# Optimization experiments

Hardware: AMD Instinct MI355X
Metric: run time of the kernel (lower is better)

## Reference

```python
import jax, jax.numpy as jnp
import numpy as np

B, N, FOV = 64, 128, 9
CH = [3, 32, 64, 128]
FLAT = CH[-1] * FOV * FOV  # 10368
ENC = 128
K = 3
G1, G2 = 128, 128
A = 5
EPS = 1e-5


def setup_inputs() -> dict:
    key = jax.random.key(0)
    ks = jax.random.split(key, 24)
    d = {}
    d["states"] = jax.random.normal(ks[0], (B, N, 3, FOV, FOV), jnp.float32)
    d["gso"] = jax.random.uniform(ks[1], (B, N, N), jnp.float32)
    i = 2
    for l in range(3):
        cin, cout = CH[l], CH[l + 1]
        d[f"c{l+1}_w"] = jax.random.normal(ks[i], (cout, cin, 3, 3), jnp.float32) * 0.05; i += 1
        d[f"c{l+1}_b"] = jnp.zeros((cout,), jnp.float32)
        d[f"c{l+1}_g"] = jnp.ones((cout,), jnp.float32)
        d[f"c{l+1}_be"] = jnp.zeros((cout,), jnp.float32)
    d["enc_w"] = jax.random.normal(ks[i], (ENC, FLAT), jnp.float32) * (1.0 / np.sqrt(FLAT)); i += 1
    d["enc_b"] = jnp.zeros((ENC,), jnp.float32)
    d["g1_w"] = jax.random.normal(ks[i], (K, G1, ENC), jnp.float32) * (1.0 / np.sqrt(ENC * K)); i += 1
    d["g1_b"] = jnp.zeros((G1,), jnp.float32)
    d["g2_w"] = jax.random.normal(ks[i], (K, G2, G1), jnp.float32) * (1.0 / np.sqrt(G1 * K)); i += 1
    d["g2_b"] = jnp.zeros((G2,), jnp.float32)
    d["act_w"] = jax.random.normal(ks[i], (A, G2), jnp.float32) * (1.0 / np.sqrt(G2)); i += 1
    d["act_b"] = jnp.zeros((A,), jnp.float32)
    return d


def _conv_bn_relu(x, w, b, gamma, beta):
    # 3x3, stride 1, padding 1 -> SAME; NCHW/OIHW
    y = jax.lax.conv_general_dilated(
        x, w, window_strides=(1, 1), padding="SAME",
        dimension_numbers=("NCHW", "OIHW", "NCHW"))
    y = y + b[None, :, None, None]
    # BatchNorm2d in training mode: batch statistics over (N, H, W)
    mu = jnp.mean(y, axis=(0, 2, 3), keepdims=True)
    var = jnp.var(y, axis=(0, 2, 3), keepdims=True)
    y = (y - mu) * jax.lax.rsqrt(var + EPS)
    y = y * gamma[None, :, None, None] + beta[None, :, None, None]
    return jax.nn.relu(y)


def _graph_filter(x, S, w, b):
    # x: [B, F, N], S: [B, N, N], w: [K, G, F] -> y = sum_k W_k (x S^k) + b
    out = jnp.einsum("bfn,gf->bgn", x, w[0])
    xk = x
    for k in range(1, w.shape[0]):
        xk = jnp.einsum("bfn,bnm->bfm", xk, S)
        out = out + jnp.einsum("bfn,gf->bgn", xk, w[k])
    return out + b[None, :, None]


def reference(states, gso,
              c1_w, c1_b, c1_g, c1_be,
              c2_w, c2_b, c2_g, c2_be,
              c3_w, c3_b, c3_g, c3_be,
              enc_w, enc_b, g1_w, g1_b, g2_w, g2_b, act_w, act_b):
    x = states.reshape(B * N, 3, FOV, FOV)
    x = _conv_bn_relu(x, c1_w, c1_b, c1_g, c1_be)
    x = _conv_bn_relu(x, c2_w, c2_b, c2_g, c2_be)
    x = _conv_bn_relu(x, c3_w, c3_b, c3_g, c3_be)
    x = x.reshape(B * N, FLAT)
    x = x @ enc_w.T + enc_b                    # [B*N, ENC]
    x = x.reshape(B, N, ENC).transpose(0, 2, 1)  # [B, F, N]
    x = jax.nn.relu(_graph_filter(x, gso, g1_w, g1_b))
    x = jax.nn.relu(_graph_filter(x, gso, g2_w, g2_b))
    x = x.transpose(0, 2, 1).reshape(B * N, G2)
    logits = x @ act_w.T + act_b
    return logits.reshape(B, N, A)
```

## Files before the change

kernel.cpp:

```cpp
#include <hip/hip_runtime.h>
#include <hip/hip_bf16.h>
#include <stdint.h>


#define NIMG 8192
#define NPIX 81
#define FLAT 10368

typedef __hip_bfloat16 bf16;
typedef short bf16x8 __attribute__((ext_vector_type(8)));
typedef float f32x4 __attribute__((ext_vector_type(4)));

__device__ __forceinline__ float bflo(unsigned u) { return __uint_as_float(u << 16); }
__device__ __forceinline__ float bfhi(unsigned u) { return __uint_as_float(u & 0xffff0000u); }
__device__ __forceinline__ unsigned short f2bf(float f) {
    unsigned u = __float_as_uint(f);
    return (unsigned short)((u + 0x7fff + ((u >> 16) & 1)) >> 16);
}

__device__ __forceinline__ bf16x8 bn8(bf16x8 a, const float* sc, const float* sh) {
    union U { bf16x8 v; unsigned u[4]; } in, out;
    in.v = a;
#pragma unroll
    for (int d = 0; d < 4; d++) {
        float lo = fmaxf(fmaf(bflo(in.u[d]), sc[2 * d],     sh[2 * d]),     0.f);
        float hi = fmaxf(fmaf(bfhi(in.u[d]), sc[2 * d + 1], sh[2 * d + 1]), 0.f);
        out.u[d] = (unsigned)f2bf(lo) | ((unsigned)f2bf(hi) << 16);
    }
    return out.v;
}

__global__ void fill_sentinel(float* __restrict__ out, int n) {
    int i = blockIdx.x * 256 + threadIdx.x;
    if (i < n) out[i] = 1.0e9f;
}

__global__ void prep_w(const float* __restrict__ c1w, const float* __restrict__ c2w,
                       const float* __restrict__ c3w,
                       float* __restrict__ w1t, bf16* __restrict__ w2m,
                       bf16* __restrict__ w3m) {
    int i0 = blockIdx.x * blockDim.x + threadIdx.x;
    int stride = gridDim.x * blockDim.x;
    for (int i = i0; i < 27 * 32; i += stride) w1t[i] = c1w[(i & 31) * 27 + (i >> 5)];
    for (int i = i0; i < 64 * 288; i += stride) {
        int oc = i / 288, r = i - oc * 288, t = r >> 5, ci = r & 31;
        w2m[i] = __float2bfloat16(c2w[oc * 288 + ci * 9 + t]);
    }
    for (int i = i0; i < 128 * 576; i += stride) {
        int oc = i / 576, r = i - oc * 576, t = r >> 6, ci = r & 63;
        w3m[i] = __float2bfloat16(c3w[oc * 576 + ci * 9 + t]);
    }
}

__global__ void prep_enc(const float* __restrict__ encw, bf16* __restrict__ ewb) {
    int i0 = blockIdx.x * blockDim.x + threadIdx.x;
    int stride = gridDim.x * blockDim.x;
    for (int i = i0; i < 128 * FLAT; i += stride) {
        int e = i / FLAT, r = i - e * FLAT;
        int kk = r >> 5, c32 = r & 31;
        int px = kk >> 2, cc = kk & 3;
        ewb[i] = __float2bfloat16(encw[(size_t)e * FLAT + (cc * 32 + c32) * 81 + px]);
    }
}

template <int NCH>
__global__ __launch_bounds__(256) void bnrelu_k(bf16* __restrict__ x,
        const float* __restrict__ st, int n8) {
    int i0 = blockIdx.x * 256 + threadIdx.x;
    int stride = gridDim.x * 256;
    for (int i = i0; i < n8; i += stride) {
        size_t base = (size_t)i * 8;
        int ch = (int)((base >> 18) & (unsigned)(NCH - 1));
        int c0 = ch * 32 + (int)(base & 31);
        float sc[8], sh[8];
#pragma unroll
        for (int j = 0; j < 8; j++) {
            sc[j] = st[c0 + j];
            sh[j] = st[NCH * 32 + c0 + j];
        }
        bf16x8 v = *(bf16x8*)(x + base);
        *(bf16x8*)(x + base) = bn8(v, sc, sh);
    }
}

__device__ __forceinline__ void load_row(const float* __restrict__ p, float* r) {
    float4 a = *(const float4*)p;
    float4 b = *(const float4*)(p + 4);
    float4 c = *(const float4*)(p + 8);
    r[0]=a.x; r[1]=a.y; r[2]=a.z;  r[3]=a.w;
    r[4]=b.x; r[5]=b.y; r[6]=b.z;  r[7]=b.w;
    r[8]=c.x; r[9]=c.y; r[10]=c.z; r[11]=c.w;
}

__device__ __forceinline__ void conv_body(const float* __restrict__ inp,
                                          const float* __restrict__ wv, float* acc) {
    float rb[3][12];
    load_row(inp, rb[0]);
    load_row(inp + 12, rb[1]);
#pragma unroll
    for (int oy = 0; oy < 9; oy++) {
        load_row(inp + (oy + 2) * 12, rb[(oy + 2) % 3]);
#pragma unroll
        for (int ky = 0; ky < 3; ky++) {
            const float* r = rb[(oy + ky) % 3];
#pragma unroll
            for (int ox = 0; ox < 9; ox++) {
                float s = acc[oy * 9 + ox];
                s = fmaf(r[ox + 0], wv[ky * 3 + 0], s);
                s = fmaf(r[ox + 1], wv[ky * 3 + 1], s);
                s = fmaf(r[ox + 2], wv[ky * 3 + 2], s);
                acc[oy * 9 + ox] = s;
            }
        }
    }
}

__global__ __launch_bounds__(128) void conv1_kernel(const float* __restrict__ xin,
        const float* __restrict__ wt, const float* __restrict__ bias,
        bf16* __restrict__ xout, float* __restrict__ sacc) {
    __shared__ __align__(16) float lds[4 * 3 * 132];
    __shared__ float Sl[128], Ql[128];
    int t = threadIdx.x;
    int img0 = blockIdx.x * 4;
    for (int i = t; i < 4 * 3 * 132; i += 128) lds[i] = 0.f;
    __syncthreads();
    const float* src = xin + (size_t)img0 * 243;
    for (int i = t; i < 4 * 243; i += 128) {
        int il = i / 243, rem = i - il * 243;
        int ci = rem / 81, px = rem - ci * 81;
        lds[(il * 3 + ci) * 132 + (px / 9 + 1) * 12 + (px % 9) + 1] = src[i];
    }
    __syncthreads();
    int oc = t & 31, il = t >> 5;
    const float* base = lds + il * 3 * 132;
    float acc[81];
    float bb = bias[oc];
#pragma unroll
    for (int i = 0; i < 81; i++) acc[i] = bb;
#pragma unroll
    for (int ci = 0; ci < 3; ci++) {
        float wv[9];
#pragma unroll
        for (int k = 0; k < 9; k++) wv[k] = wt[(ci * 9 + k) * 32 + oc];
        conv_body(base + ci * 132, wv, acc);
    }
    bf16* dst = xout + (size_t)(img0 + il) * 32 + oc;
    const size_t PXS = (size_t)NIMG * 32;
    float s = 0.f, q = 0.f;
#pragma unroll
    for (int p = 0; p < 81; p++) {
        float v = acc[p];
        s += v; q = fmaf(v, v, q);
        dst[p * PXS] = __float2bfloat16(v);
    }
    Sl[il * 32 + oc] = s;
    Ql[il * 32 + oc] = q;
    __syncthreads();
    if (t < 32)
        atomicAdd(&sacc[t], Sl[t] + Sl[32 + t] + Sl[64 + t] + Sl[96 + t]);
    else if (t < 64) {
        int c = t - 32;
        atomicAdd(&sacc[32 + c], Ql[c] + Ql[32 + c] + Ql[64 + c] + Ql[96 + c]);
    }
}

template <int CI, int COT, int OCS>
__global__ __launch_bounds__(256, (CI == 64) ? 2 : 4) void conv_tile(
        const bf16* __restrict__ xin,
        const bf16* __restrict__ wm, const float* __restrict__ bias,
        bf16* __restrict__ xout, float* __restrict__ sacc) {
    constexpr int NCH = CI / 32;
    constexpr int NCHO = COT / 32;
    constexpr int NOC = COT / OCS;
    constexpr int NF = NOC / 16;
    constexpr int LNF = (NF == 8) ? 3 : 2;
    constexpr int ROW = 9 * CI;
    constexpr int STEPS = 9 * NCH;
    constexpr int PHASES = STEPS / 9;
    constexpr int HS = STEPS / PHASES;
    constexpr size_t CSTRIDE = (size_t)NIMG * 32;
    __shared__ bf16 Bs[HS * NF * 64 * 8];
    __shared__ float Ss[2][4][NOC];

    const int lin = blockIdx.x;
    const int xcd = lin & 7;
    const int slot = lin >> 3;
    constexpr int PSL = 81 * OCS;
    const int igl = slot / PSL;
    const int rem = slot - igl * PSL;
    const int p = rem / OCS;
    const int ob = rem - p * OCS;
    const int ig = xcd * 4 + igl;
    const int oc0 = ob * NOC;
    const int py = p / 9, pxx = p - py * 9;
    const int tid = threadIdx.x;
    const int lane = tid & 63, wv = tid >> 6;
    const int m = lane & 15, quad = lane >> 4;
    const long img0 = (long)ig * 256 + wv * 64;

    int qt[9]; bool vt[9];
#pragma unroll
    for (int t = 0; t < 9; t++) {
        int iy = py + t / 3 - 1, ix = pxx + (t % 3) - 1;
        vt[t] = ((unsigned)iy < 9u) && ((unsigned)ix < 9u);
        qt[t] = vt[t] ? iy * 9 + ix : p;
    }

    f32x4 acc[4][NF];
#pragma unroll
    for (int nf = 0; nf < NF; nf++) {
        float bb = bias[oc0 + nf * 16 + m];
#pragma unroll
        for (int ms = 0; ms < 4; ms++) {
            acc[ms][nf][0] = bb; acc[ms][nf][1] = bb;
            acc[ms][nf][2] = bb; acc[ms][nf][3] = bb;
        }
    }
    const bf16* ab[4];
#pragma unroll
    for (int ms = 0; ms < 4; ms++)
        ab[ms] = xin + (img0 + ms * 16 + m) * 32 + quad * 8;

    const bf16* bsl = &Bs[lane * 8];

#pragma unroll
    for (int ph = 0; ph < PHASES; ph++) {
        __syncthreads();
        for (int i = tid; i < HS * NF * 64; i += 256) {
            int l2 = i & 63, nf = (i >> 6) & (NF - 1), sl = i >> (6 + LNF);
            int s = ph * HS + sl;
            int t = s / NCH, ch = s - t * NCH;
            int mm = l2 & 15, qq = l2 >> 4;
            *(bf16x8*)(&Bs[(size_t)i * 8]) =
                *(const bf16x8*)(wm + (size_t)(oc0 + nf * 16 + mm) * ROW + t * CI + ch * 32 + qq * 8);
        }
        __syncthreads();
#pragma unroll
        for (int sl = 0; sl < HS; sl++) {
            const int s = ph * HS + sl;
            const int t = s / NCH, ch = s - t * NCH;
            if (vt[t]) {
                bf16x8 bfr[NF];
#pragma unroll
                for (int nf = 0; nf < NF; nf++)
                    bfr[nf] = *(const bf16x8*)(bsl + (sl * NF + nf) * 512);
                bf16x8 a[4];
#pragma unroll
                for (int ms = 0; ms < 4; ms++)
                    a[ms] = *(const bf16x8*)(ab[ms] + (size_t)(qt[t] * NCH + ch) * CSTRIDE);
#pragma unroll
                for (int ms = 0; ms < 4; ms++) {
#pragma unroll
                    for (int nf = 0; nf < NF; nf++)
                        acc[ms][nf] = __builtin_amdgcn_mfma_f32_16x16x32_bf16(a[ms], bfr[nf], acc[ms][nf], 0, 0, 0);
                }
            }
        }
    }

    const int och = oc0 >> 5;
#pragma unroll
    for (int ms = 0; ms < 4; ms++)
#pragma unroll
        for (int nf = 0; nf < NF; nf++) {
            bf16* orow = xout
                + (((size_t)p * NCHO + och + (nf >> 1)) * NIMG + img0 + ms * 16 + quad * 4) * 32
                + (nf & 1) * 16 + m;
#pragma unroll
            for (int r = 0; r < 4; r++)
                orow[r * 32] = __float2bfloat16(acc[ms][nf][r]);
        }

    float ssum[NF], sq[NF];
#pragma unroll
    for (int nf = 0; nf < NF; nf++) {
        float s = 0.f, q = 0.f;
#pragma unroll
        for (int ms = 0; ms < 4; ms++)
#pragma unroll
            for (int r = 0; r < 4; r++) {
                float v = acc[ms][nf][r];
                s += v; q = fmaf(v, v, q);
            }
        s += __shfl_xor(s, 16); s += __shfl_xor(s, 32);
        q += __shfl_xor(q, 16); q += __shfl_xor(q, 32);
        ssum[nf] = s; sq[nf] = q;
    }
    if (lane < 16) {
#pragma unroll
        for (int nf = 0; nf < NF; nf++) {
            Ss[0][wv][nf * 16 + lane] = ssum[nf];
            Ss[1][wv][nf * 16 + lane] = sq[nf];
        }
    }
    __syncthreads();
    if (tid < NOC) {
        float a = Ss[0][0][tid] + Ss[0][1][tid] + Ss[0][2][tid] + Ss[0][3][tid];
        atomicAdd(&sacc[oc0 + tid], a);
    } else if (tid < 2 * NOC) {
        int c = tid - NOC;
        float a = Ss[1][0][c] + Ss[1][1][c] + Ss[1][2][c] + Ss[1][3][c];
        atomicAdd(&sacc[COT + oc0 + c], a);
    }
}

__global__ __launch_bounds__(256) void enc_mfma(const bf16* __restrict__ x3,
        const bf16* __restrict__ ewb, const float* __restrict__ st,
        float* __restrict__ part) {
    const int lin = blockIdx.x;
    const int xcd = lin & 7;
    const int slot = lin >> 3;
    const int igl = slot >> 3;
    const int combo = slot & 7;
    const int ks = combo >> 1, nh = combo & 1;
    const int ig = xcd * 8 + igl;
    const int lane = threadIdx.x & 63, wv = threadIdx.x >> 6;
    const int m = lane & 15, quad = lane >> 4;
    const long img0 = (long)ig * 128 + wv * 32;
    constexpr size_t CSTRIDE = (size_t)NIMG * 32;

    float scv[4][8], shv[4][8];
#pragma unroll
    for (int cc = 0; cc < 4; cc++)
#pragma unroll
        for (int j = 0; j < 8; j++) {
            int ci = cc * 32 + quad * 8 + j;
            scv[cc][j] = st[ci];
            shv[cc][j] = st[128 + ci];
        }

    f32x4 acc[2][4];
#pragma unroll
    for (int ms = 0; ms < 2; ms++)
#pragma unroll
        for (int nf = 0; nf < 4; nf++) {
            acc[ms][nf][0]=0.f; acc[ms][nf][1]=0.f; acc[ms][nf][2]=0.f; acc[ms][nf][3]=0.f;
        }
    const bf16* ab[2];
    const bf16* bb[4];
#pragma unroll
    for (int ms = 0; ms < 2; ms++)
        ab[ms] = x3 + (size_t)(ks * 81) * CSTRIDE + (img0 + ms * 16 + m) * 32 + quad * 8;
#pragma unroll
    for (int nf = 0; nf < 4; nf++)
        bb[nf] = ewb + (size_t)(nh * 64 + nf * 16 + m) * FLAT + ks * 81 * 32 + quad * 8;

#pragma unroll 3
    for (int c = 0; c < 81; c++) {
        const int cc = (ks + c) & 3;
        bf16x8 Ac[2], Bc[4];
#pragma unroll
        for (int ms = 0; ms < 2; ms++) {
            bf16x8 raw = *(const bf16x8*)(ab[ms] + (size_t)c * CSTRIDE);
            Ac[ms] = bn8(raw, scv[cc], shv[cc]);
        }
#pragma unroll
        for (int nf = 0; nf < 4; nf++) Bc[nf] = *(const bf16x8*)(bb[nf] + c * 32);
#pragma unroll
        for (int nf = 0; nf < 4; nf++)
#pragma unroll
            for (int ms = 0; ms < 2; ms++)
                acc[ms][nf] = __builtin_amdgcn_mfma_f32_16x16x32_bf16(Ac[ms], Bc[nf], acc[ms][nf], 0, 0, 0);
    }

    float* pp = part + (size_t)ks * (NIMG * 128) + (img0 + quad * 4) * 128 + nh * 64 + m;
#pragma unroll
    for (int ms = 0; ms < 2; ms++)
#pragma unroll
        for (int nf = 0; nf < 4; nf++)
#pragma unroll
            for (int r = 0; r < 4; r++)
                pp[(ms * 16 + r) * 128 + nf * 16] = acc[ms][nf][r];
}

template <int CO>
__global__ void stats_fin(const float* __restrict__ acc, const float* __restrict__ gamma,
                          const float* __restrict__ beta, float* __restrict__ st) {
    int c = threadIdx.x;
    if (c < CO) {
        const float inv = 1.0f / (8192.0f * 81.0f);
        float m = acc[c] * inv;
        float var = acc[CO + c] * inv - m * m;
        float istd = rsqrtf(var + 1e-5f);
        float sc = istd * gamma[c];
        st[c] = sc;
        st[CO + c] = beta[c] - m * sc;
    }
}

__global__ void enc_reduce(const float* __restrict__ part, const float* __restrict__ encb,
                           float* __restrict__ xT) {
    int i = blockIdx.x * 256 + threadIdx.x;
    const int NP = NIMG * 128;
    if (i < NP) {
        float v = part[i] + part[NP + i] + part[2 * NP + i] + part[3 * NP + i] + encb[i & 127];
        int img = i >> 7, f = i & 127;
        xT[(size_t)(img >> 7) * 16384 + f * 128 + (img & 127)] = v;
    }
}

__global__ __launch_bounds__(256) void mm_xs(const float* __restrict__ A,
        const float* __restrict__ S, float* __restrict__ Y) {
    __shared__ __align__(16) float Sc[32 * 132];
    __shared__ float Acm[32 * 33];
    int b = blockIdx.y, f0 = blockIdx.x * 32;
    int t = threadIdx.x;
    int fl = t & 31, mg = t >> 5;
    const float* Ab = A + (size_t)b * 16384;
    const float* Sb = S + (size_t)b * 16384;
    float acc[16];
#pragma unroll
    for (int j = 0; j < 16; j++) acc[j] = 0.f;
    for (int nc = 0; nc < 128; nc += 32) {
#pragma unroll
        for (int r = 0; r < 4; r++) {
            int i4 = r * 256 + t;
            int nn = i4 >> 5, m4 = (i4 & 31) * 4;
            *(float4*)&Sc[nn * 132 + m4] = *(const float4*)&Sb[(size_t)(nc + nn) * 128 + m4];
        }
#pragma unroll
        for (int r = 0; r < 4; r++) {
            int i = r * 256 + t;
            int ff = i >> 5, nn = i & 31;
            Acm[ff * 33 + nn] = Ab[(size_t)(f0 + ff) * 128 + nc + nn];
        }
        __syncthreads();
#pragma unroll 4
        for (int nn = 0; nn < 32; nn++) {
            float a = Acm[fl * 33 + nn];
#pragma unroll
            for (int j = 0; j < 4; j++) {
                float4 s4 = *(const float4*)&Sc[nn * 132 + mg * 16 + j * 4];
                acc[j*4+0] = fmaf(a, s4.x, acc[j*4+0]);
                acc[j*4+1] = fmaf(a, s4.y, acc[j*4+1]);
                acc[j*4+2] = fmaf(a, s4.z, acc[j*4+2]);
                acc[j*4+3] = fmaf(a, s4.w, acc[j*4+3]);
            }
        }
        __syncthreads();
    }
    float* yb = Y + (size_t)b * 16384 + (size_t)(f0 + fl) * 128 + mg * 16;
#pragma unroll
    for (int j = 0; j < 4; j++)
        *(float4*)&yb[j * 4] = make_float4(acc[j*4], acc[j*4+1], acc[j*4+2], acc[j*4+3]);
}

__global__ __launch_bounds__(256) void gf_combine(const float* __restrict__ Z0,
        const float* __restrict__ Z1, const float* __restrict__ Z2,
        const float* __restrict__ W, const float* __restrict__ bias,
        float* __restrict__ out) {
    __shared__ __align__(16) float Zc[32 * 132];
    __shared__ float Wc[32 * 33];
    int b = blockIdx.y, g0 = blockIdx.x * 32;
    int t = threadIdx.x;
    int gl = t & 31, mg = t >> 5;
    float acc[16];
    float bb = bias[g0 + gl];
#pragma unroll
    for (int j = 0; j < 16; j++) acc[j] = bb;
    const float* Zs[3] = {Z0 + (size_t)b * 16384, Z1 + (size_t)b * 16384, Z2 + (size_t)b * 16384};
    for (int j3 = 0; j3 < 3; j3++) {
        const float* Zb = Zs[j3];
        const float* Wj = W + j3 * 16384;
        for (int fc = 0; fc < 128; fc += 32) {
#pragma unroll
            for (int r = 0; r < 4; r++) {
                int i4 = r * 256 + t;
                int ff = i4 >> 5, m4 = (i4 & 31) * 4;
                *(float4*)&Zc[ff * 132 + m4] = *(const float4*)&Zb[(size_t)(fc + ff) * 128 + m4];
            }
#pragma unroll
            for (int r = 0; r < 4; r++) {
                int i = r * 256 + t;
                int gg = i >> 5, ff = i & 31;
                Wc[gg * 33 + ff] = Wj[(size_t)(g0 + gg) * 128 + fc + ff];
            }
            __syncthreads();
#pragma unroll 4
            for (int ff = 0; ff < 32; ff++) {
                float w = Wc[gl * 33 + ff];
#pragma unroll
                for (int j = 0; j < 4; j++) {
                    float4 z4 = *(const float4*)&Zc[ff * 132 + mg * 16 + j * 4];
                    acc[j*4+0] = fmaf(w, z4.x, acc[j*4+0]);
                    acc[j*4+1] = fmaf(w, z4.y, acc[j*4+1]);
                    acc[j*4+2] = fmaf(w, z4.z, acc[j*4+2]);
                    acc[j*4+3] = fmaf(w, z4.w, acc[j*4+3]);
                }
            }
            __syncthreads();
        }
    }
    float* ob = out + (size_t)b * 16384 + (size_t)(g0 + gl) * 128 + mg * 16;
#pragma unroll
    for (int j = 0; j < 4; j++)
        *(float4*)&ob[j * 4] = make_float4(fmaxf(acc[j*4], 0.f), fmaxf(acc[j*4+1], 0.f),
                                           fmaxf(acc[j*4+2], 0.f), fmaxf(acc[j*4+3], 0.f));
}

__global__ __launch_bounds__(128) void act_kernel(const float* __restrict__ X,
        const float* __restrict__ aw, const float* __restrict__ ab,
        float* __restrict__ out) {
    int b = blockIdx.x, n = threadIdx.x;
    float acc[5];
#pragma unroll
    for (int a = 0; a < 5; a++) acc[a] = ab[a];
    const float* xb = X + (size_t)b * 16384 + n;
#pragma unroll 4
    for (int g = 0; g < 128; g++) {
        float v = xb[(size_t)g * 128];
#pragma unroll
        for (int a = 0; a < 5; a++) acc[a] = fmaf(v, aw[a * 128 + g], acc[a]);
    }
    float* ob = out + ((size_t)b * 128 + n) * 5;
#pragma unroll
    for (int a = 0; a < 5; a++) ob[a] = acc[a];
}

extern "C" void kernel_launch(void* const* d_in, const int* in_sizes, int n_in,
                              void* d_out, int out_size, void* d_ws, size_t ws_size,
                              hipStream_t stream) {
    const float* states = (const float*)d_in[0];
    const float* gso    = (const float*)d_in[1];
    const float* c1w  = (const float*)d_in[2];
    const float* c1b  = (const float*)d_in[3];
    const float* c1g  = (const float*)d_in[4];
    const float* c1be = (const float*)d_in[5];
    const float* c2w  = (const float*)d_in[6];
    const float* c2b  = (const float*)d_in[7];
    const float* c2g  = (const float*)d_in[8];
    const float* c2be = (const float*)d_in[9];
    const float* c3w  = (const float*)d_in[10];
    const float* c3b  = (const float*)d_in[11];
    const float* c3g  = (const float*)d_in[12];
    const float* c3be = (const float*)d_in[13];
    const float* encw = (const float*)d_in[14];
    const float* encb = (const float*)d_in[15];
    const float* g1w  = (const float*)d_in[16];
    const float* g1b  = (const float*)d_in[17];
    const float* g2w  = (const float*)d_in[18];
    const float* g2b  = (const float*)d_in[19];
    const float* aw   = (const float*)d_in[20];
    const float* ab   = (const float*)d_in[21];
    float* out = (float*)d_out;
    char* ws = (char*)d_ws;

    size_t o = 0;
    auto take = [&](size_t bytes) { size_t r = o; o += (bytes + 255) & ~(size_t)255; return r; };
    const size_t o_x3  = take((size_t)81 * 4 * NIMG * 32 * 2);
    const size_t o_x2  = take((size_t)81 * 2 * NIMG * 32 * 2);
    const size_t o_w1t = take(27 * 32 * 4);
    const size_t o_w2m = take(64 * 288 * 2);
    const size_t o_w3m = take(128 * 576 * 2);
    const size_t o_acc = take(448 * 4);
    const size_t o_st1 = take(2 * 32 * 4);
    const size_t o_st2 = take(2 * 64 * 4);
    const size_t o_st3 = take(2 * 128 * 4);
    if (ws_size < o) {
        fill_sentinel<<<(out_size + 255) / 256, 256, 0, stream>>>(out, out_size);
        return;
    }

    const size_t o_x1 = o_x3;
    const size_t o_ewb  = o_x2;
    const size_t o_part = o_x2 + 2654208;
    const size_t o_xT   = o_part + 16777216;
    const size_t o_y1   = o_xT + 4194304;
    const size_t o_y2   = o_y1 + 4194304;
    const size_t o_G1   = o_y2 + 4194304;
    const size_t o_G2   = o_G1 + 4194304;

    bf16* x1 = (bf16*)(ws + o_x1);
    bf16* x2 = (bf16*)(ws + o_x2);
    bf16* x3 = (bf16*)(ws + o_x3);
    float* w1t = (float*)(ws + o_w1t);
    bf16* w2m = (bf16*)(ws + o_w2m);
    bf16* w3m = (bf16*)(ws + o_w3m);
    float* acc1 = (float*)(ws + o_acc);
    float* acc2 = acc1 + 64;
    float* acc3 = acc1 + 192;
    float* st1 = (float*)(ws + o_st1);
    float* st2 = (float*)(ws + o_st2);
    float* st3 = (float*)(ws + o_st3);
    bf16* ewb = (bf16*)(ws + o_ewb);
    float* partp = (float*)(ws + o_part);
    float* xT = (float*)(ws + o_xT);
    float* y1 = (float*)(ws + o_y1);
    float* y2 = (float*)(ws + o_y2);
    float* xG1 = (float*)(ws + o_G1);
    float* xG2 = (float*)(ws + o_G2);

    hipMemsetAsync(ws + o_acc, 0, 448 * 4, stream);
    prep_w<<<128, 256, 0, stream>>>(c1w, c2w, c3w, w1t, w2m, w3m);

    conv1_kernel<<<2048, 128, 0, stream>>>(states, w1t, c1b, x1, acc1);
    stats_fin<32><<<1, 32, 0, stream>>>(acc1, c1g, c1be, st1);
    bnrelu_k<1><<<4096, 256, 0, stream>>>(x1, st1, 81 * 1 * NIMG * 32 / 8);

    conv_tile<32, 64, 1><<<2592, 256, 0, stream>>>(x1, w2m, c2b, x2, acc2);
    stats_fin<64><<<1, 64, 0, stream>>>(acc2, c2g, c2be, st2);
    bnrelu_k<2><<<4096, 256, 0, stream>>>(x2, st2, 81 * 2 * NIMG * 32 / 8);

    conv_tile<64, 128, 1><<<2592, 256, 0, stream>>>(x2, w3m, c3b, x3, acc3);
    stats_fin<128><<<1, 128, 0, stream>>>(acc3, c3g, c3be, st3);

    prep_enc<<<2048, 256, 0, stream>>>(encw, ewb);
    enc_mfma<<<512, 256, 0, stream>>>(x3, ewb, st3, partp);
    enc_reduce<<<4096, 256, 0, stream>>>(partp, encb, xT);

    mm_xs<<<dim3(4, 64), 256, 0, stream>>>(xT, gso, y1);
    mm_xs<<<dim3(4, 64), 256, 0, stream>>>(y1, gso, y2);
    gf_combine<<<dim3(4, 64), 256, 0, stream>>>(xT, y1, y2, g1w, g1b, xG1);

    mm_xs<<<dim3(4, 64), 256, 0, stream>>>(xG1, gso, y1);
    mm_xs<<<dim3(4, 64), 256, 0, stream>>>(y1, gso, y2);
    gf_combine<<<dim3(4, 64), 256, 0, stream>>>(xG1, y1, y2, g2w, g2b, xG2);

    act_kernel<<<64, 128, 0, stream>>>(xG2, aw, ab, out);
}
```

Baseline: 687.8 us.

## Fold BN stats finalize into consumers, retile encoder MFMA and graph matmuls

Removes the three single-block stats_fin launches by computing BN scale/shift inside bnrelu_k (via shared memory) and inside enc_mfma per thread. Retiles enc_mfma so each wave covers 16 images across all 128 output features instead of 32 images by 64 features, which drops the nh split. Halves the feature tile in mm_xs and gf_combine so twice as many blocks launch (512 instead of 256), aiming for better CU occupancy on small graph stages. The trade-off is redundant stats computation in every block and more B-operand loads per A load in the encoder.

```diff
diff --git a/kernel.cpp b/kernel.cpp
--- a/kernel.cpp
+++ b/kernel.cpp
@@ -65,8 +65,20 @@
 
 template <int NCH>
 __global__ __launch_bounds__(256) void bnrelu_k(bf16* __restrict__ x,
-        const float* __restrict__ st, int n8) {
-    int i0 = blockIdx.x * 256 + threadIdx.x;
+        const float* __restrict__ accp, const float* __restrict__ gma,
+        const float* __restrict__ bta, int n8) {
+    __shared__ float stl[2][NCH * 32];
+    int t = threadIdx.x;
+    if (t < NCH * 32) {
+        const float inv = 1.0f / (8192.0f * 81.0f);
+        float mean = accp[t] * inv;
+        float var = accp[NCH * 32 + t] * inv - mean * mean;
+        float sc = rsqrtf(var + 1e-5f) * gma[t];
+        stl[0][t] = sc;
+        stl[1][t] = bta[t] - mean * sc;
+    }
+    __syncthreads();
+    int i0 = blockIdx.x * 256 + t;
     int stride = gridDim.x * 256;
     for (int i = i0; i < n8; i += stride) {
         size_t base = (size_t)i * 8;
@@ -75,8 +87,8 @@
         float sc[8], sh[8];
 #pragma unroll
         for (int j = 0; j < 8; j++) {
-            sc[j] = st[c0 + j];
-            sh[j] = st[NCH * 32 + c0 + j];
+            sc[j] = stl[0][c0 + j];
+            sh[j] = stl[1][c0 + j];
         }
         bf16x8 v = *(bf16x8*)(x + base);
         *(bf16x8*)(x + base) = bn8(v, sc, sh);
@@ -305,87 +317,64 @@
 }
 
 __global__ __launch_bounds__(256) void enc_mfma(const bf16* __restrict__ x3,
-        const bf16* __restrict__ ewb, const float* __restrict__ st,
+        const bf16* __restrict__ ewb, const float* __restrict__ acc3,
+        const float* __restrict__ gma, const float* __restrict__ bta,
         float* __restrict__ part) {
     const int lin = blockIdx.x;
     const int xcd = lin & 7;
     const int slot = lin >> 3;
-    const int igl = slot >> 3;
-    const int combo = slot & 7;
-    const int ks = combo >> 1, nh = combo & 1;
-    const int ig = xcd * 8 + igl;
+    const int igl = slot >> 2;
+    const int ks = slot & 3;
+    const int ig = xcd * 16 + igl;
     const int lane = threadIdx.x & 63, wv = threadIdx.x >> 6;
     const int m = lane & 15, quad = lane >> 4;
-    const long img0 = (long)ig * 128 + wv * 32;
+    const long img0 = (long)ig * 64 + wv * 16;
     constexpr size_t CSTRIDE = (size_t)NIMG * 32;
 
+    const float inv = 1.0f / (8192.0f * 81.0f);
     float scv[4][8], shv[4][8];
 #pragma unroll
     for (int cc = 0; cc < 4; cc++)
 #pragma unroll
         for (int j = 0; j < 8; j++) {
             int ci = cc * 32 + quad * 8 + j;
-            scv[cc][j] = st[ci];
-            shv[cc][j] = st[128 + ci];
-        }
-
-    f32x4 acc[2][4];
-#pragma unroll
-    for (int ms = 0; ms < 2; ms++)
-#pragma unroll
-        for (int nf = 0; nf < 4; nf++) {
-            acc[ms][nf][0]=0.f; acc[ms][nf][1]=0.f; acc[ms][nf][2]=0.f; acc[ms][nf][3]=0.f;
-        }
-    const bf16* ab[2];
-    const bf16* bb[4];
-#pragma unroll
-    for (int ms = 0; ms < 2; ms++)
-        ab[ms] = x3 + (size_t)(ks * 81) * CSTRIDE + (img0 + ms * 16 + m) * 32 + quad * 8;
-#pragma unroll
-    for (int nf = 0; nf < 4; nf++)
-        bb[nf] = ewb + (size_t)(nh * 64 + nf * 16 + m) * FLAT + ks * 81 * 32 + quad * 8;
+            float mean = acc3[ci] * inv;
+            float var = acc3[128 + ci] * inv - mean * mean;
+            float sc = rsqrtf(var + 1e-5f) * gma[ci];
+            scv[cc][j] = sc;
+            shv[cc][j] = bta[ci] - mean * sc;
+        }
+
+    f32x4 acc[8];
+#pragma unroll
+    for (int nf = 0; nf < 8; nf++) {
+        acc[nf][0]=0.f; acc[nf][1]=0.f; acc[nf][2]=0.f; acc[nf][3]=0.f;
+    }
+    const bf16* ab = x3 + (size_t)(ks * 81) * CSTRIDE + (img0 + m) * 32 + quad * 8;
+    const bf16* bb[8];
+#pragma unroll
+    for (int nf = 0; nf < 8; nf++)
+        bb[nf] = ewb + (size_t)(nf * 16 + m) * FLAT + ks * 81 * 32 + quad * 8;
 
 #pragma unroll 3
     for (int c = 0; c < 81; c++) {
         const int cc = (ks + c) & 3;
-        bf16x8 Ac[2], Bc[4];
-#pragma unroll
-        for (int ms = 0; ms < 2; ms++) {
-            bf16x8 raw = *(const bf16x8*)(ab[ms] + (size_t)c * CSTRIDE);
-            Ac[ms] = bn8(raw, scv[cc], shv[cc]);
-        }
-#pragma unroll
-        for (int nf = 0; nf < 4; nf++) Bc[nf] = *(const bf16x8*)(bb[nf] + c * 32);
-#pragma unroll
-        for (int nf = 0; nf < 4; nf++)
-#pragma unroll
-            for (int ms = 0; ms < 2; ms++)
-                acc[ms][nf] = __builtin_amdgcn_mfma_f32_16x16x32_bf16(Ac[ms], Bc[nf], acc[ms][nf], 0, 0, 0);
-    }
-
-    float* pp = part + (size_t)ks * (NIMG * 128) + (img0 + quad * 4) * 128 + nh * 64 + m;
-#pragma unroll
-    for (int ms = 0; ms < 2; ms++)
-#pragma unroll
-        for (int nf = 0; nf < 4; nf++)
-#pragma unroll
-            for (int r = 0; r < 4; r++)
-                pp[(ms * 16 + r) * 128 + nf * 16] = acc[ms][nf][r];
-}
-
-template <int CO>
-__global__ void stats_fin(const float* __restrict__ acc, const float* __restrict__ gamma,
-                          const float* __restrict__ beta, float* __restrict__ st) {
-    int c = threadIdx.x;
-    if (c < CO) {
-        const float inv = 1.0f / (8192.0f * 81.0f);
-        float m = acc[c] * inv;
-        float var = acc[CO + c] * inv - m * m;
-        float istd = rsqrtf(var + 1e-5f);
-        float sc = istd * gamma[c];
-        st[c] = sc;
-        st[CO + c] = beta[c] - m * sc;
-    }
+        bf16x8 raw = *(const bf16x8*)(ab + (size_t)c * CSTRIDE);
+        bf16x8 Ac = bn8(raw, scv[cc], shv[cc]);
+        bf16x8 Bc[8];
+#pragma unroll
+        for (int nf = 0; nf < 8; nf++) Bc[nf] = *(const bf16x8*)(bb[nf] + c * 32);
+#pragma unroll
+        for (int nf = 0; nf < 8; nf++)
+            acc[nf] = __builtin_amdgcn_mfma_f32_16x16x32_bf16(Ac, Bc[nf], acc[nf], 0, 0, 0);
+    }
+
+    float* pp = part + (size_t)ks * (NIMG * 128) + (img0 + quad * 4) * 128 + m;
+#pragma unroll
+    for (int nf = 0; nf < 8; nf++)
+#pragma unroll
+        for (int r = 0; r < 4; r++)
+            pp[r * 128 + nf * 16] = acc[nf][r];
 }
 
 __global__ void enc_reduce(const float* __restrict__ part, const float* __restrict__ encb,
@@ -402,15 +391,15 @@
 __global__ __launch_bounds__(256) void mm_xs(const float* __restrict__ A,
         const float* __restrict__ S, float* __restrict__ Y) {
     __shared__ __align__(16) float Sc[32 * 132];
-    __shared__ float Acm[32 * 33];
-    int b = blockIdx.y, f0 = blockIdx.x * 32;
+    __shared__ float Acm[16 * 33];
+    int b = blockIdx.y, f0 = blockIdx.x * 16;
     int t = threadIdx.x;
-    int fl = t & 31, mg = t >> 5;
+    int fl = t & 15, mg = t >> 4;
     const float* Ab = A + (size_t)b * 16384;
     const float* Sb = S + (size_t)b * 16384;
-    float acc[16];
-#pragma unroll
-    for (int j = 0; j < 16; j++) acc[j] = 0.f;
+    float acc[8];
+#pragma unroll
+    for (int j = 0; j < 8; j++) acc[j] = 0.f;
     for (int nc = 0; nc < 128; nc += 32) {
 #pragma unroll
         for (int r = 0; r < 4; r++) {
@@ -419,7 +408,7 @@
             *(float4*)&Sc[nn * 132 + m4] = *(const float4*)&Sb[(size_t)(nc + nn) * 128 + m4];
         }
 #pragma unroll
-        for (int r = 0; r < 4; r++) {
+        for (int r = 0; r < 2; r++) {
             int i = r * 256 + t;
             int ff = i >> 5, nn = i & 31;
             Acm[ff * 33 + nn] = Ab[(size_t)(f0 + ff) * 128 + nc + nn];
@@ -429,8 +418,8 @@
         for (int nn = 0; nn < 32; nn++) {
             float a = Acm[fl * 33 + nn];
 #pragma unroll
-            for (int j = 0; j < 4; j++) {
-                float4 s4 = *(const float4*)&Sc[nn * 132 + mg * 16 + j * 4];
+            for (int j = 0; j < 2; j++) {
+                float4 s4 = *(const float4*)&Sc[nn * 132 + mg * 8 + j * 4];
                 acc[j*4+0] = fmaf(a, s4.x, acc[j*4+0]);
                 acc[j*4+1] = fmaf(a, s4.y, acc[j*4+1]);
                 acc[j*4+2] = fmaf(a, s4.z, acc[j*4+2]);
@@ -439,10 +428,9 @@
         }
         __syncthreads();
     }
-    float* yb = Y + (size_t)b * 16384 + (size_t)(f0 + fl) * 128 + mg * 16;
-#pragma unroll
-    for (int j = 0; j < 4; j++)
-        *(float4*)&yb[j * 4] = make_float4(acc[j*4], acc[j*4+1], acc[j*4+2], acc[j*4+3]);
+    float* yb = Y + (size_t)b * 16384 + (size_t)(f0 + fl) * 128 + mg * 8;
+    *(float4*)&yb[0] = make_float4(acc[0], acc[1], acc[2], acc[3]);
+    *(float4*)&yb[4] = make_float4(acc[4], acc[5], acc[6], acc[7]);
 }
 
 __global__ __launch_bounds__(256) void gf_combine(const float* __restrict__ Z0,
@@ -450,14 +438,14 @@
         const float* __restrict__ W, const float* __restrict__ bias,
         float* __restrict__ out) {
     __shared__ __align__(16) float Zc[32 * 132];
-    __shared__ float Wc[32 * 33];
-    int b = blockIdx.y, g0 = blockIdx.x * 32;
+    __shared__ float Wc[16 * 33];
+    int b = blockIdx.y, g0 = blockIdx.x * 16;
     int t = threadIdx.x;
-    int gl = t & 31, mg = t >> 5;
-    float acc[16];
+    int gl = t & 15, mg = t >> 4;
+    float acc[8];
     float bb = bias[g0 + gl];
 #pragma unroll
-    for (int j = 0; j < 16; j++) acc[j] = bb;
+    for (int j = 0; j < 8; j++) acc[j] = bb;
     const float* Zs[3] = {Z0 + (size_t)b * 16384, Z1 + (size_t)b * 16384, Z2 + (size_t)b * 16384};
     for (int j3 = 0; j3 < 3; j3++) {
         const float* Zb = Zs[j3];
@@ -470,7 +458,7 @@
                 *(float4*)&Zc[ff * 132 + m4] = *(const float4*)&Zb[(size_t)(fc + ff) * 128 + m4];
             }
 #pragma unroll
-            for (int r = 0; r < 4; r++) {
+            for (int r = 0; r < 2; r++) {
                 int i = r * 256 + t;
                 int gg = i >> 5, ff = i & 31;
                 Wc[gg * 33 + ff] = Wj[(size_t)(g0 + gg) * 128 + fc + ff];
@@ -480,8 +468,8 @@
             for (int ff = 0; ff < 32; ff++) {
                 float w = Wc[gl * 33 + ff];
 #pragma unroll
-                for (int j = 0; j < 4; j++) {
-                    float4 z4 = *(const float4*)&Zc[ff * 132 + mg * 16 + j * 4];
+                for (int j = 0; j < 2; j++) {
+                    float4 z4 = *(const float4*)&Zc[ff * 132 + mg * 8 + j * 4];
                     acc[j*4+0] = fmaf(w, z4.x, acc[j*4+0]);
                     acc[j*4+1] = fmaf(w, z4.y, acc[j*4+1]);
                     acc[j*4+2] = fmaf(w, z4.z, acc[j*4+2]);
@@ -491,11 +479,11 @@
             __syncthreads();
         }
     }
-    float* ob = out + (size_t)b * 16384 + (size_t)(g0 + gl) * 128 + mg * 16;
-#pragma unroll
-    for (int j = 0; j < 4; j++)
-        *(float4*)&ob[j * 4] = make_float4(fmaxf(acc[j*4], 0.f), fmaxf(acc[j*4+1], 0.f),
-                                           fmaxf(acc[j*4+2], 0.f), fmaxf(acc[j*4+3], 0.f));
+    float* ob = out + (size_t)b * 16384 + (size_t)(g0 + gl) * 128 + mg * 8;
+    *(float4*)&ob[0] = make_float4(fmaxf(acc[0], 0.f), fmaxf(acc[1], 0.f),
+                                   fmaxf(acc[2], 0.f), fmaxf(acc[3], 0.f));
+    *(float4*)&ob[4] = make_float4(fmaxf(acc[4], 0.f), fmaxf(acc[5], 0.f),
+                                   fmaxf(acc[6], 0.f), fmaxf(acc[7], 0.f));
 }
 
 __global__ __launch_bounds__(128) void act_kernel(const float* __restrict__ X,
@@ -553,9 +541,6 @@
     const size_t o_w2m = take(64 * 288 * 2);
     const size_t o_w3m = take(128 * 576 * 2);
     const size_t o_acc = take(448 * 4);
-    const size_t o_st1 = take(2 * 32 * 4);
-    const size_t o_st2 = take(2 * 64 * 4);
-    const size_t o_st3 = take(2 * 128 * 4);
     if (ws_size < o) {
         fill_sentinel<<<(out_size + 255) / 256, 256, 0, stream>>>(out, out_size);
         return;
@@ -579,9 +564,6 @@
     float* acc1 = (float*)(ws + o_acc);
     float* acc2 = acc1 + 64;
     float* acc3 = acc1 + 192;
-    float* st1 = (float*)(ws + o_st1);
-    float* st2 = (float*)(ws + o_st2);
-    float* st3 = (float*)(ws + o_st3);
     bf16* ewb = (bf16*)(ws + o_ewb);
     float* partp = (float*)(ws + o_part);
     float* xT = (float*)(ws + o_xT);
@@ -594,27 +576,24 @@
     prep_w<<<128, 256, 0, stream>>>(c1w, c2w, c3w, w1t, w2m, w3m);
 
     conv1_kernel<<<2048, 128, 0, stream>>>(states, w1t, c1b, x1, acc1);
-    stats_fin<32><<<1, 32, 0, stream>>>(acc1, c1g, c1be, st1);
-    bnrelu_k<1><<<4096, 256, 0, stream>>>(x1, st1, 81 * 1 * NIMG * 32 / 8);
+    bnrelu_k<1><<<4096, 256, 0, stream>>>(x1, acc1, c1g, c1be, 81 * 1 * NIMG * 32 / 8);
 
     conv_tile<32, 64, 1><<<2592, 256, 0, stream>>>(x1, w2m, c2b, x2, acc2);
-    stats_fin<64><<<1, 64, 0, stream>>>(acc2, c2g, c2be, st2);
-    bnrelu_k<2><<<4096, 256, 0, stream>>>(x2, st2, 81 * 2 * NIMG * 32 / 8);
+    bnrelu_k<2><<<4096, 256, 0, stream>>>(x2, acc2, c2g, c2be, 81 * 2 * NIMG * 32 / 8);
 
     conv_tile<64, 128, 1><<<2592, 256, 0, stream>>>(x2, w3m, c3b, x3, acc3);
-    stats_fin<128><<<1, 128, 0, stream>>>(acc3, c3g, c3be, st3);
 
     prep_enc<<<2048, 256, 0, stream>>>(encw, ewb);
-    enc_mfma<<<512, 256, 0, stream>>>(x3, ewb, st3, partp);
+    enc_mfma<<<512, 256, 0, stream>>>(x3, ewb, acc3, c3g, c3be, partp);
     enc_reduce<<<4096, 256, 0, stream>>>(partp, encb, xT);
 
-    mm_xs<<<dim3(4, 64), 256, 0, stream>>>(xT, gso, y1);
-    mm_xs<<<dim3(4, 64), 256, 0, stream>>>(y1, gso, y2);
-    gf_combine<<<dim3(4, 64), 256, 0, stream>>>(xT, y1, y2, g1w, g1b, xG1);
-
-    mm_xs<<<dim3(4, 64), 256, 0, stream>>>(xG1, gso, y1);
-    mm_xs<<<dim3(4, 64), 256, 0, stream>>>(y1, gso, y2);
-    gf_combine<<<dim3(4, 64), 256, 0, stream>>>(xG1, y1, y2, g2w, g2b, xG2);
+    mm_xs<<<dim3(8, 64), 256, 0, stream>>>(xT, gso, y1);
+    mm_xs<<<dim3(8, 64), 256, 0, stream>>>(y1, gso, y2);
+    gf_combine<<<dim3(8, 64), 256, 0, stream>>>(xT, y1, y2, g1w, g1b, xG1);
+
+    mm_xs<<<dim3(8, 64), 256, 0, stream>>>(xG1, gso, y1);
+    mm_xs<<<dim3(8, 64), 256, 0, stream>>>(y1, gso, y2);
+    gf_combine<<<dim3(8, 64), 256, 0, stream>>>(xG1, y1, y2, g2w, g2b, xG2);
 
     act_kernel<<<64, 128, 0, stream>>>(xG2, aw, ab, out);
 }
```

Measured after the change: 723.9 us. +5.3%, slower.
